# Performance work log

Measured on AMD Instinct MI355X. Metric: run time of the kernel, lower is better.

Reference implementation:

```python
import jax, jax.numpy as jnp
import numpy as np

N_ATOMS, N_BONDS, B = 3072, 12288, 64
D, H, L = 256, 8, 4
AF, BF = 74, 12
HD = D // H
EPS = 1e-5


def layer_norm(x, g, b):
    m = jnp.mean(x, -1, keepdims=True)
    v = jnp.mean((x - m) ** 2, -1, keepdims=True)
    return (x - m) / jnp.sqrt(v + EPS) * g + b


def mha(x, in_w, in_b, out_w, out_b, mask=None):
    # torch nn.MultiheadAttention with packed in_proj, batch of 1 sequence
    n = x.shape[0]
    qkv = x @ in_w.T + in_b                      # [n, 3D]
    q, k, v = jnp.split(qkv, 3, axis=-1)
    q = q.reshape(n, H, HD)
    k = k.reshape(n, H, HD)
    v = v.reshape(n, H, HD)
    scores = jnp.einsum('qhd,khd->hqk', q, k) / jnp.asarray(np.sqrt(HD), x.dtype)
    if mask is not None:
        scores = jnp.where(mask[None], scores, jnp.asarray(-1e9, x.dtype))
    att = jax.nn.softmax(scores, axis=-1)
    out = jnp.einsum('hqk,khd->qhd', att, v).reshape(n, D)
    return out @ out_w.T + out_b


def setup_inputs() -> dict:
    key = jax.random.key(0)
    ks = jax.random.split(key, 12)
    s = 0.05
    return {
        'atom_features': jax.random.normal(ks[0], (N_ATOMS, AF), jnp.float32),
        'bond_features': jax.random.normal(ks[1], (N_BONDS, BF), jnp.float32),
        'edge_indices': jax.random.randint(ks[2], (2, N_BONDS), 0, N_ATOMS),
        'batch_idx': jnp.sort(jax.random.randint(ks[3], (N_ATOMS,), 0, B)),
        'atom_w': jax.random.normal(ks[4], (D, AF), jnp.float32) * s,
        'atom_b': jnp.zeros((D,), jnp.float32),
        'bond_w': jax.random.normal(ks[5], (D, BF), jnp.float32) * s,
        'bond_b': jnp.zeros((D,), jnp.float32),
        'conv_w': jax.random.normal(ks[6], (L, D, 2 * D), jnp.float32) * s,
        'conv_b': jnp.zeros((L, D), jnp.float32),
        'attn_in_w': jax.random.normal(ks[7], (L, 3 * D, D), jnp.float32) * s,
        'attn_in_b': jnp.zeros((L, 3 * D), jnp.float32),
        'attn_out_w': jax.random.normal(ks[8], (L, D, D), jnp.float32) * s,
        'attn_out_b': jnp.zeros((L, D), jnp.float32),
        'ln_g': jnp.ones((L, D), jnp.float32),
        'ln_b': jnp.zeros((L, D), jnp.float32),
        'gattn_in_w': jax.random.normal(ks[9], (3 * D, D), jnp.float32) * s,
        'gattn_in_b': jnp.zeros((3 * D,), jnp.float32),
        'gattn_out_w': jax.random.normal(ks[10], (D, D), jnp.float32) * s,
        'gattn_out_b': jnp.zeros((D,), jnp.float32),
        'gn_g': jnp.ones((D,), jnp.float32),
        'gn_b': jnp.zeros((D,), jnp.float32),
    }


def reference(atom_features, bond_features, edge_indices, batch_idx,
              atom_w, atom_b, bond_w, bond_b, conv_w, conv_b,
              attn_in_w, attn_in_b, attn_out_w, attn_out_b, ln_g, ln_b,
              gattn_in_w, gattn_in_b, gattn_out_w, gattn_out_b, gn_g, gn_b):
    atom_h = atom_features @ atom_w.T + atom_b       # [N, D]
    bond_h = bond_features @ bond_w.T + bond_b       # [E, D]
    src, tgt = edge_indices[0], edge_indices[1]
    for i in range(L):
        # gather -> concat -> linear -> relu -> scatter-add
        messages = jnp.concatenate([atom_h[src] + bond_h, atom_h[tgt]], axis=-1)
        messages = jax.nn.relu(messages @ conv_w[i].T + conv_b[i])
        aggregated = jnp.zeros_like(atom_h).at[tgt].add(messages)
        # self-attention over all atoms as a single sequence (as in source)
        attended = mha(atom_h, attn_in_w[i], attn_in_b[i], attn_out_w[i], attn_out_b[i])
        atom_h = layer_norm(atom_h + aggregated + attended, ln_g[i], ln_b[i])
    # per-graph pooled attention == full attention masked to same-graph pairs
    same_graph = batch_idx[:, None] == batch_idx[None, :]
    pooled = mha(atom_h, gattn_in_w, gattn_in_b, gattn_out_w, gattn_out_b, mask=same_graph)
    pooled = layer_norm(pooled, gn_g, gn_b)
    sums = jax.ops.segment_sum(pooled, batch_idx, num_segments=B)
    counts = jax.ops.segment_sum(jnp.ones((pooled.shape[0],), pooled.dtype), batch_idx, num_segments=B)
    return sums / jnp.maximum(counts, 1.0)[:, None]   # empty graphs -> zeros, as in source
```

## Files before the change

### kernel.cpp

```cpp
#include <hip/hip_runtime.h>
#include <hip/hip_bf16.h>
#include <math.h>

#define NATOMS 3072
#define NBONDS 12288
#define NGRAPH 64
#define DIM 256
#define NH 8
#define HDIM 32
#define NLAYER 4
#define AFD 74
#define BFD 12
#define LNEPS 1e-5f
#define HSZ (NATOMS * HDIM)

typedef __attribute__((ext_vector_type(8))) short bf16x8;
typedef __attribute__((ext_vector_type(4))) short s16x4;
typedef __attribute__((ext_vector_type(4))) float f32x4;

static __device__ __forceinline__ short f2bf(float x) {
  union { float f; unsigned u; } v; v.f = x;
  unsigned r = v.u + 0x7fff + ((v.u >> 16) & 1);
  return (short)(r >> 16);
}

static __device__ __forceinline__ size_t afrag(int m, int c) {
  return ((size_t)(m >> 4) * 8 + (c >> 5)) * 512 + (m & 15) * 32 + (c & 31);
}

__global__ __launch_bounds__(256) void repack_w_kernel(
    const float* __restrict__ W, short* __restrict__ out, int kcShift, int n8) {
  const int o8 = blockIdx.x * 256 + threadIdx.x;
  if (o8 >= n8) return;
  const int g = o8 & 3, lq = (o8 >> 2) & 15, sub = (o8 >> 6) & 3;
  const int chunk = o8 >> 8;
  const int kc = chunk & ((1 << kcShift) - 1);
  const int nt = chunk >> kcShift;
  const int K = 32 << kcShift;
  const int n = nt * 64 + sub * 16 + lq;
  const int c = kc * 32 + g * 8;
  const float* src = W + (size_t)n * K + c;
  bf16x8 o;
  #pragma unroll
  for (int j = 0; j < 8; ++j) o[j] = f2bf(src[j]);
  ((bf16x8*)out)[o8] = o;
}

__global__ __launch_bounds__(256) void atom_proj_kernel(
    const float* __restrict__ feat, const float* __restrict__ w,
    const float* __restrict__ b, float* __restrict__ out, short* __restrict__ outbf) {
  __shared__ float x[AFD];
  const int a = blockIdx.x, t = threadIdx.x;
  if (t < AFD) x[t] = feat[a * AFD + t];
  __syncthreads();
  float acc = b[t];
  const float* wr = w + t * AFD;
  for (int k = 0; k < AFD; ++k) acc = fmaf(wr[k], x[k], acc);
  out[a * DIM + t] = acc;
  outbf[afrag(a, t)] = f2bf(acc);
}

__global__ __launch_bounds__(256) void bond_proj_kernel(
    const float* __restrict__ feat, const float* __restrict__ w,
    const float* __restrict__ b, short* __restrict__ outbf) {
  __shared__ float x[BFD];
  const int e = blockIdx.x, t = threadIdx.x;
  if (t < BFD) x[t] = feat[e * BFD + t];
  __syncthreads();
  float acc = b[t];
  const float* wr = w + t * BFD;
  #pragma unroll
  for (int k = 0; k < BFD; ++k) acc = fmaf(wr[k], x[k], acc);
  outbf[afrag(e, t)] = f2bf(acc);
}

__global__ __launch_bounds__(256) void hist_kernel(
    const int* __restrict__ tgt, int* __restrict__ counts) {
  const int e = blockIdx.x * 256 + threadIdx.x;
  if (e < NBONDS) atomicAdd(&counts[tgt[e]], 1);
}

__global__ __launch_bounds__(256) void scan_kernel(
    const int* __restrict__ counts, int* __restrict__ rowptr,
    int* __restrict__ cursor) {
  __shared__ int part[256];
  const int t = threadIdx.x;
  int loc[12], s = 0;
  #pragma unroll
  for (int j = 0; j < 12; ++j) { loc[j] = counts[t * 12 + j]; s += loc[j]; }
  part[t] = s;
  __syncthreads();
  for (int o = 1; o < 256; o <<= 1) {
    const int v = (t >= o) ? part[t - o] : 0;
    __syncthreads();
    part[t] += v;
    __syncthreads();
  }
  int running = part[t] - s;
  #pragma unroll
  for (int j = 0; j < 12; ++j) {
    rowptr[t * 12 + j] = running;
    cursor[t * 12 + j] = running;
    running += loc[j];
  }
  if (t == 255) rowptr[NATOMS] = running;
}

__global__ __launch_bounds__(256) void scatter_kernel(
    const int* __restrict__ tgt, int* __restrict__ cursor,
    int* __restrict__ elist) {
  const int e = blockIdx.x * 256 + threadIdx.x;
  if (e < NBONDS) {
    const int pos = atomicAdd(&cursor[tgt[e]], 1);
    elist[pos] = e;
  }
}

__global__ __launch_bounds__(256) void msg_csr_kernel(
    const float* __restrict__ G1, const float* __restrict__ B1,
    const float* __restrict__ G2, const float* __restrict__ bias,
    const int* __restrict__ src, const int* __restrict__ rowptr,
    const int* __restrict__ elist, float* __restrict__ agg) {
  const int wv = threadIdx.x >> 6, lane = threadIdx.x & 63;
  const int t = blockIdx.x * 4 + wv;
  const int c = lane * 4;
  const float4 bb = *(const float4*)&bias[c];
  const float4 g2 = *(const float4*)&G2[(size_t)t * DIM + c];
  const float gx = g2.x + bb.x, gy = g2.y + bb.y, gz = g2.z + bb.z, gw = g2.w + bb.w;
  float4 acc = make_float4(0.f, 0.f, 0.f, 0.f);
  const int beg = rowptr[t], end = rowptr[t + 1];
  for (int j = beg; j < end; ++j) {
    const int e = elist[j];
    const int s = src[e];
    const float4 g1 = *(const float4*)&G1[(size_t)s * DIM + c];
    const float4 b1 = *(const float4*)&B1[(size_t)e * DIM + c];
    acc.x += fmaxf(g1.x + b1.x + gx, 0.f);
    acc.y += fmaxf(g1.y + b1.y + gy, 0.f);
    acc.z += fmaxf(g1.z + b1.z + gz, 0.f);
    acc.w += fmaxf(g1.w + b1.w + gw, 0.f);
  }
  *(float4*)&agg[(size_t)t * DIM + c] = acc;
}

template <int KCS, int KCB>
__global__ __launch_bounds__(256) void gemm_bt_kernel(
    const short* __restrict__ A, const short* __restrict__ W,
    const float* __restrict__ bias, float* __restrict__ Cf,
    short* __restrict__ Cbf, int ldc, short* __restrict__ Qb,
    short* __restrict__ Kff, short* __restrict__ Vtf, float qscale) {
  const int t = threadIdx.x;
  const int w = t >> 6, l = t & 63;
  const int lq = l & 15, g = l >> 4;
  const int mrow = blockIdx.x * 32 + (w & 1) * 16 + lq;
  const int nbase = blockIdx.y * 128 + (w >> 1) * 64;
  const int lof = lq * 32 + g * 8;
  const short* arow = A + (size_t)(mrow >> 4) * 8 * 512 + lof;
  const short* wch = W + ((size_t)(nbase >> 6) * KCS + KCB) * 2048 + lof;

  bf16x8 Xall[8];
  #pragma unroll
  for (int kc = 0; kc < 8; ++kc) Xall[kc] = *(const bf16x8*)(arow + kc * 512);

  bf16x8 Wb[2][4];
  #pragma unroll
  for (int sub = 0; sub < 4; ++sub)
    Wb[0][sub] = *(const bf16x8*)(wch + sub * 512);

  f32x4 acc[4] = {{0.f,0.f,0.f,0.f},{0.f,0.f,0.f,0.f},{0.f,0.f,0.f,0.f},{0.f,0.f,0.f,0.f}};
  #pragma unroll
  for (int kc = 0; kc < 8; ++kc) {
    const int cur = kc & 1, nxt = cur ^ 1;
    if (kc < 7) {
      #pragma unroll
      for (int sub = 0; sub < 4; ++sub)
        Wb[nxt][sub] = *(const bf16x8*)(wch + (kc + 1) * 2048 + sub * 512);
    }
    __builtin_amdgcn_sched_barrier(0);
    #pragma unroll
    for (int sub = 0; sub < 4; ++sub)
      acc[sub] = __builtin_amdgcn_mfma_f32_16x16x32_bf16(Wb[cur][sub], Xall[kc], acc[sub], 0, 0, 0);
  }

  const bool qkvmode = (Qb != nullptr);
  #pragma unroll
  for (int sub = 0; sub < 4; ++sub) {
    const int n = nbase + sub * 16 + g * 4;
    float4 v = make_float4(acc[sub][0], acc[sub][1], acc[sub][2], acc[sub][3]);
    if (bias) {
      const float4 b4 = *(const float4*)&bias[n];
      v.x += b4.x; v.y += b4.y; v.z += b4.z; v.w += b4.w;
    }
    if (qkvmode) {
      const int key = mrow;
      if (n < 256) {
        s16x4 o;
        o[0] = f2bf(v.x * qscale); o[1] = f2bf(v.y * qscale);
        o[2] = f2bf(v.z * qscale); o[3] = f2bf(v.w * qscale);
        *(s16x4*)&Qb[afrag(mrow, n)] = o;
      } else if (n < 512) {
        const int d = n - 256, h = d >> 5, dd = d & 31;
        const size_t base = (size_t)h * HSZ + (size_t)(key >> 6) * 2048 +
                            (size_t)((key & 63) >> 4) * 512 +
                            ((dd >> 3) * 16 + (key & 15)) * 8 + (dd & 7);
        s16x4 o;
        o[0] = f2bf(v.x); o[1] = f2bf(v.y); o[2] = f2bf(v.z); o[3] = f2bf(v.w);
        *(s16x4*)&Kff[base] = o;
      } else {
        const int d = n - 512, h = d >> 5;
        const int kt = (key & 63) >> 5, gg = (key & 31) >> 3, j = key & 7;
        const int hh = (d & 31) >> 4;
        const size_t base = (size_t)h * HSZ + (size_t)(key >> 6) * 2048 +
                            (size_t)(kt * 2 + hh) * 512 + gg * 128 + j;
        Vtf[base + (size_t)((d + 0) & 15) * 8] = f2bf(v.x);
        Vtf[base + (size_t)((d + 1) & 15) * 8] = f2bf(v.y);
        Vtf[base + (size_t)((d + 2) & 15) * 8] = f2bf(v.z);
        Vtf[base + (size_t)((d + 3) & 15) * 8] = f2bf(v.w);
      }
    } else {
      if (Cf) *(float4*)&Cf[(size_t)mrow * ldc + n] = v;
      if (Cbf) {
        s16x4 o;
        o[0] = f2bf(v.x); o[1] = f2bf(v.y); o[2] = f2bf(v.z); o[3] = f2bf(v.w);
        *(s16x4*)&Cbf[afrag(mrow, n)] = o;
      }
    }
  }
}

__global__ __launch_bounds__(256) void gemm_dual_kernel(
    const short* __restrict__ A, const short* __restrict__ W,
    float* __restrict__ G1, float* __restrict__ G2) {
  const int t = threadIdx.x;
  const int w = t >> 6, l = t & 63;
  const int lq = l & 15, g = l >> 4;
  const int mrow = blockIdx.x * 32 + (w & 1) * 16 + lq;
  const int nbase = blockIdx.y * 128 + (w >> 1) * 64;
  const int half = nbase >> 8;
  const int nl = nbase & 255;
  const int lof = lq * 32 + g * 8;
  const short* arow = A + (size_t)(mrow >> 4) * 8 * 512 + lof;
  const short* wch = W + ((size_t)(nl >> 6) * 16 + half * 8) * 2048 + lof;

  bf16x8 Xall[8];
  #pragma unroll
  for (int kc = 0; kc < 8; ++kc) Xall[kc] = *(const bf16x8*)(arow + kc * 512);

  bf16x8 Wb[2][4];
  #pragma unroll
  for (int sub = 0; sub < 4; ++sub)
    Wb[0][sub] = *(const bf16x8*)(wch + sub * 512);

  f32x4 acc[4] = {{0.f,0.f,0.f,0.f},{0.f,0.f,0.f,0.f},{0.f,0.f,0.f,0.f},{0.f,0.f,0.f,0.f}};
  #pragma unroll
  for (int kc = 0; kc < 8; ++kc) {
    const int cur = kc & 1, nxt = cur ^ 1;
    if (kc < 7) {
      #pragma unroll
      for (int sub = 0; sub < 4; ++sub)
        Wb[nxt][sub] = *(const bf16x8*)(wch + (kc + 1) * 2048 + sub * 512);
    }
    __builtin_amdgcn_sched_barrier(0);
    #pragma unroll
    for (int sub = 0; sub < 4; ++sub)
      acc[sub] = __builtin_amdgcn_mfma_f32_16x16x32_bf16(Wb[cur][sub], Xall[kc], acc[sub], 0, 0, 0);
  }

  float* C = half ? G2 : G1;
  #pragma unroll
  for (int sub = 0; sub < 4; ++sub) {
    const int n = nl + sub * 16 + g * 4;
    *(float4*)&C[(size_t)mrow * DIM + n] =
        make_float4(acc[sub][0], acc[sub][1], acc[sub][2], acc[sub][3]);
  }
}

template <bool RESID>
__global__ __launch_bounds__(256) void outproj_ln_kernel(
    const short* __restrict__ A, const short* __restrict__ W,
    const float* __restrict__ bias, const float* __restrict__ r1,
    const float* __restrict__ r2, const float* __restrict__ g,
    const float* __restrict__ b, float* __restrict__ outf,
    short* __restrict__ outbf) {
  __shared__ float Red[4][2][16];
  const int t = threadIdx.x;
  const int w = t >> 6, l = t & 63;
  const int lq = l & 15, gg = l >> 4;
  const int mtile = blockIdx.x;
  const int mrow = mtile * 16 + lq;
  const int nbase = w * 64;
  const int lof = lq * 32 + gg * 8;
  const short* arow = A + (size_t)mtile * 8 * 512 + lof;
  const short* wch = W + ((size_t)(nbase >> 6) * 8) * 2048 + lof;

  bf16x8 Xall[8];
  #pragma unroll
  for (int kc = 0; kc < 8; ++kc) Xall[kc] = *(const bf16x8*)(arow + kc * 512);

  bf16x8 Wb[2][4];
  #pragma unroll
  for (int sub = 0; sub < 4; ++sub)
    Wb[0][sub] = *(const bf16x8*)(wch + sub * 512);

  f32x4 acc[4] = {{0.f,0.f,0.f,0.f},{0.f,0.f,0.f,0.f},{0.f,0.f,0.f,0.f},{0.f,0.f,0.f,0.f}};
  #pragma unroll
  for (int kc = 0; kc < 8; ++kc) {
    const int cur = kc & 1, nxt = cur ^ 1;
    if (kc < 7) {
      #pragma unroll
      for (int sub = 0; sub < 4; ++sub)
        Wb[nxt][sub] = *(const bf16x8*)(wch + (kc + 1) * 2048 + sub * 512);
    }
    __builtin_amdgcn_sched_barrier(0);
    #pragma unroll
    for (int sub = 0; sub < 4; ++sub)
      acc[sub] = __builtin_amdgcn_mfma_f32_16x16x32_bf16(Wb[cur][sub], Xall[kc], acc[sub], 0, 0, 0);
  }

  float y[4][4];
  float sp = 0.f, qp = 0.f;
  #pragma unroll
  for (int sub = 0; sub < 4; ++sub) {
    const int n = nbase + sub * 16 + gg * 4;
    const float4 b4 = *(const float4*)&bias[n];
    float4 v = make_float4(acc[sub][0] + b4.x, acc[sub][1] + b4.y,
                           acc[sub][2] + b4.z, acc[sub][3] + b4.w);
    if (RESID) {
      const size_t idx = (size_t)mrow * DIM + n;
      const float4 a4 = *(const float4*)&r1[idx];
      const float4 c4 = *(const float4*)&r2[idx];
      v.x += a4.x + c4.x; v.y += a4.y + c4.y;
      v.z += a4.z + c4.z; v.w += a4.w + c4.w;
    }
    y[sub][0] = v.x; y[sub][1] = v.y; y[sub][2] = v.z; y[sub][3] = v.w;
    sp += (v.x + v.y) + (v.z + v.w);
    qp += (v.x * v.x + v.y * v.y) + (v.z * v.z + v.w * v.w);
  }
  sp += __shfl_xor(sp, 16); sp += __shfl_xor(sp, 32);
  qp += __shfl_xor(qp, 16); qp += __shfl_xor(qp, 32);
  if (l < 16) { Red[w][0][lq] = sp; Red[w][1][lq] = qp; }
  __syncthreads();
  const float s = Red[0][0][lq] + Red[1][0][lq] + Red[2][0][lq] + Red[3][0][lq];
  const float q = Red[0][1][lq] + Red[1][1][lq] + Red[2][1][lq] + Red[3][1][lq];
  const float mean = s * (1.f / 256.f);
  const float var = q * (1.f / 256.f) - mean * mean;
  const float rstd = rsqrtf(var + LNEPS);

  #pragma unroll
  for (int sub = 0; sub < 4; ++sub) {
    const int n = nbase + sub * 16 + gg * 4;
    const float4 g4 = *(const float4*)&g[n];
    const float4 b4 = *(const float4*)&b[n];
    float4 o;
    o.x = (y[sub][0] - mean) * rstd * g4.x + b4.x;
    o.y = (y[sub][1] - mean) * rstd * g4.y + b4.y;
    o.z = (y[sub][2] - mean) * rstd * g4.z + b4.z;
    o.w = (y[sub][3] - mean) * rstd * g4.w + b4.w;
    if (outf) *(float4*)&outf[(size_t)mrow * DIM + n] = o;
    if (outbf) {
      s16x4 ob;
      ob[0] = f2bf(o.x); ob[1] = f2bf(o.y); ob[2] = f2bf(o.z); ob[3] = f2bf(o.w);
      *(s16x4*)&outbf[afrag(mrow, n)] = ob;
    }
  }
}

template <bool MASKED>
__global__ __launch_bounds__(256) void attn_mfma_kernel(
    const short* __restrict__ Qb, const short* __restrict__ Kff,
    const short* __restrict__ Vtf, const int* __restrict__ bidx,
    short* __restrict__ outbf) {
  __shared__ short Ps[4][2][16 * 72];
  __shared__ float Comb[3][64][18];

  const int t = threadIdx.x;
  const int h = blockIdx.y;
  const int wid = t >> 6;
  const int l = t & 63;
  const int lq = l & 15;
  const int g = l >> 4;
  const int qt0 = blockIdx.x * 32;

  const bf16x8 Qf0 = *(const bf16x8*)(Qb + ((size_t)(qt0 >> 4) * 8 + h) * 512 + lq * 32 + g * 8);
  const bf16x8 Qf1 = *(const bf16x8*)(Qb + ((size_t)(qt0 >> 4) * 8 + 8 + h) * 512 + lq * 32 + g * 8);
  const int qg0 = MASKED ? bidx[qt0 + lq] : 0;
  const int qg1 = MASKED ? bidx[qt0 + 16 + lq] : 0;

  bf16x8 OnesF;
  #pragma unroll
  for (int j = 0; j < 8; ++j) OnesF[j] = (short)0x3F80;

  const short* kh = Kff + (size_t)h * HSZ + l * 8;
  const short* vh = Vtf + (size_t)h * HSZ + l * 8;

  f32x4 accO[2][2] = {{{0.f,0.f,0.f,0.f},{0.f,0.f,0.f,0.f}},
                      {{0.f,0.f,0.f,0.f},{0.f,0.f,0.f,0.f}}};
  f32x4 accL[2] = {{0.f,0.f,0.f,0.f},{0.f,0.f,0.f,0.f}};

  const int kbeg = wid * (NATOMS / 4);
  const int kend = kbeg + NATOMS / 4;

  bf16x8 Kf[2][4];
  bf16x8 Vf[2][4];
  int4 KBv[2][4];

#define LOAD_TILE(buf, kc)                                                      \
  {                                                                             \
    const size_t tb = (size_t)((kc) >> 6) * 2048;                               \
    _Pragma("unroll")                                                           \
    for (int kk = 0; kk < 4; ++kk)                                              \
      Kf[buf][kk] = *(const bf16x8*)(kh + tb + kk * 512);                       \
    _Pragma("unroll")                                                           \
    for (int ff = 0; ff < 4; ++ff)                                              \
      Vf[buf][ff] = *(const bf16x8*)(vh + tb + ff * 512);                       \
    if (MASKED) {                                                               \
      _Pragma("unroll")                                                         \
      for (int kk = 0; kk < 4; ++kk)                                            \
        KBv[buf][kk] = *(const int4*)(bidx + (kc) + kk * 16 + g * 4);           \
    }                                                                           \
  }

  LOAD_TILE(0, kbeg);

  for (int k0 = kbeg; k0 < kend; k0 += 128) {
    #pragma unroll
    for (int ph = 0; ph < 2; ++ph) {
      const int kcur = k0 + ph * 64;
      int kn = kcur + 64;
      if (kn >= kend) kn = kbeg;
      const int pb = ph ^ 1;
      LOAD_TILE(pb, kn);
      __builtin_amdgcn_sched_barrier(0);

      #pragma unroll
// ... 30 lines not shown
      for (int qt = 0; qt < 2; ++qt) {
        #pragma unroll
        for (int kt = 0; kt < 2; ++kt) {
          const bf16x8 Pf = *(const bf16x8*)&Ps[wid][qt][lq * 72 + kt * 32 + g * 8];
          #pragma unroll
          for (int hh = 0; hh < 2; ++hh)
            accO[qt][hh] = __builtin_amdgcn_mfma_f32_16x16x32_bf16(
                Vf[ph][kt * 2 + hh], Pf, accO[qt][hh], 0, 0, 0);
          accL[qt] = __builtin_amdgcn_mfma_f32_16x16x32_bf16(OnesF, Pf, accL[qt], 0, 0, 0);
        }
      }
    }
  }
#undef LOAD_TILE

  if (wid > 0) {
    #pragma unroll
    for (int qt = 0; qt < 2; ++qt) {
      Comb[wid - 1][l][qt * 9] = accL[qt][0];
      #pragma unroll
      for (int hh = 0; hh < 2; ++hh)
        #pragma unroll
        for (int r = 0; r < 4; ++r)
          Comb[wid - 1][l][qt * 9 + 1 + hh * 4 + r] = accO[qt][hh][r];
    }
  }
  __syncthreads();
  if (wid == 0) {
    #pragma unroll
    for (int qt = 0; qt < 2; ++qt) {
      float tot = accL[qt][0];
      #pragma unroll
      for (int w2 = 0; w2 < 3; ++w2) {
        tot += Comb[w2][l][qt * 9];
        #pragma unroll
        for (int hh = 0; hh < 2; ++hh)
          #pragma unroll
          for (int r = 0; r < 4; ++r)
            accO[qt][hh][r] += Comb[w2][l][qt * 9 + 1 + hh * 4 + r];
      }
      const float inv = 1.f / tot;
      const int qrow = qt0 + qt * 16 + lq;
      #pragma unroll
      for (int hh = 0; hh < 2; ++hh) {
        s16x4 o;
        #pragma unroll
        for (int r = 0; r < 4; ++r) o[r] = f2bf(accO[qt][hh][r] * inv);
        *(s16x4*)&outbf[afrag(qrow, h * HDIM + hh * 16 + g * 4)] = o;
      }
    }
  }
}

__global__ __launch_bounds__(256) void pool_seg_kernel(
    const float* __restrict__ pooled, const int* __restrict__ bidx,
    float* __restrict__ out) {
  const int b = blockIdx.x, t = threadIdx.x;
  __shared__ int se[2];
  if (t < 2) {
    const int target = b + t;
    int lo = 0, hi = NATOMS;
    while (lo < hi) {
      const int mid = (lo + hi) >> 1;
      if (bidx[mid] < target) lo = mid + 1; else hi = mid;
    }
    se[t] = lo;
  }
  __syncthreads();
  const int beg = se[0], end = se[1];
  float acc = 0.f;
  for (int a = beg; a < end; ++a) acc += pooled[(size_t)a * DIM + t];
  out[(size_t)b * DIM + t] = acc / fmaxf((float)(end - beg), 1.f);
}

extern "C" void kernel_launch(void* const* d_in, const int* in_sizes, int n_in,
                              void* d_out, int out_size, void* d_ws, size_t ws_size,
                              hipStream_t stream) {
  const float* atom_features = (const float*)d_in[0];
  const float* bond_features = (const float*)d_in[1];
  const int* edge_indices = (const int*)d_in[2];
  const int* batch_idx = (const int*)d_in[3];
  const float* atom_w = (const float*)d_in[4];
  const float* atom_b = (const float*)d_in[5];
  const float* bond_w = (const float*)d_in[6];
  const float* bond_b = (const float*)d_in[7];
  const float* conv_w = (const float*)d_in[8];
  const float* conv_b = (const float*)d_in[9];
  const float* attn_in_w = (const float*)d_in[10];
  const float* attn_in_b = (const float*)d_in[11];
  const float* attn_out_w = (const float*)d_in[12];
  const float* attn_out_b = (const float*)d_in[13];
  const float* ln_g = (const float*)d_in[14];
  const float* ln_b = (const float*)d_in[15];
  const float* gattn_in_w = (const float*)d_in[16];
  const float* gattn_in_b = (const float*)d_in[17];
  const float* gattn_out_w = (const float*)d_in[18];
  const float* gattn_out_b = (const float*)d_in[19];
  const float* gn_g = (const float*)d_in[20];
  const float* gn_b = (const float*)d_in[21];

  const float QSCALE = 0.17677669529663687f * 1.4426950408889634f;

  char* wsb = (char*)d_ws;
  size_t off = 0;
  auto alloc_f = [&](size_t n) { float* p = (float*)(wsb + off); off += n * 4; return p; };
  auto alloc_s = [&](size_t n) { short* p = (short*)(wsb + off); off += n * 2; return p; };
  auto alloc_i = [&](size_t n) { int* p = (int*)(wsb + off); off += n * 4; return p; };

  float* atom_h = alloc_f((size_t)NATOMS * DIM);
  float* B1     = alloc_f((size_t)NBONDS * DIM);
  float* G1     = alloc_f((size_t)NATOMS * DIM);
  float* G2     = alloc_f((size_t)NATOMS * DIM);
  float* agg    = alloc_f((size_t)NATOMS * DIM);
  short* atom_hb = alloc_s((size_t)NATOMS * DIM);
  short* bond_hb = alloc_s((size_t)NBONDS * DIM);
  short* q_b     = alloc_s((size_t)NATOMS * DIM);
  short* kff_b   = alloc_s((size_t)NATOMS * DIM);
  short* vtf_b   = alloc_s((size_t)NATOMS * DIM);
  short* att_b   = alloc_s((size_t)NATOMS * DIM);
  short* conv_wb = alloc_s((size_t)NLAYER * DIM * 2 * DIM);
  short* in_wb   = alloc_s((size_t)NLAYER * 3 * DIM * DIM);
  short* out_wb  = alloc_s((size_t)NLAYER * DIM * DIM);
  short* gin_wb  = alloc_s((size_t)3 * DIM * DIM);
  short* gout_wb = alloc_s((size_t)DIM * DIM);
  int* counts = alloc_i(NATOMS);
  int* rowptr = alloc_i(NATOMS + 1);
  int* cursor = alloc_i(NATOMS);
  int* elist  = alloc_i(NBONDS);
  if (ws_size < off) return;
  float* pooled = B1;

  const int* src = edge_indices;
  const int* tgt = edge_indices + NBONDS;

  hipMemsetAsync(counts, 0, NATOMS * sizeof(int), stream);
  hist_kernel<<<NBONDS / 256, 256, 0, stream>>>(tgt, counts);
  scan_kernel<<<1, 256, 0, stream>>>(counts, rowptr, cursor);
  scatter_kernel<<<NBONDS / 256, 256, 0, stream>>>(tgt, cursor, elist);

  auto repk = [&](const float* s, short* d, int kcShift, int N, int K) {
    const int n8 = N * K / 8;
    repack_w_kernel<<<(n8 + 255) / 256, 256, 0, stream>>>(s, d, kcShift, n8);
  };
  repk(conv_w, conv_wb, 4, NLAYER * DIM, 2 * DIM);
  repk(attn_in_w, in_wb, 3, NLAYER * 3 * DIM, DIM);
  repk(attn_out_w, out_wb, 3, NLAYER * DIM, DIM);
  repk(gattn_in_w, gin_wb, 3, 3 * DIM, DIM);
  repk(gattn_out_w, gout_wb, 3, DIM, DIM);

  atom_proj_kernel<<<NATOMS, 256, 0, stream>>>(atom_features, atom_w, atom_b, atom_h, atom_hb);
  bond_proj_kernel<<<NBONDS, 256, 0, stream>>>(bond_features, bond_w, bond_b, bond_hb);

  for (int i = 0; i < NLAYER; ++i) {
    const short* cw = conv_wb + (size_t)i * DIM * 2 * DIM;
    gemm_bt_kernel<16, 0><<<dim3(NBONDS / 32, 2), 256, 0, stream>>>(
        bond_hb, cw, nullptr, B1, nullptr, DIM, nullptr, nullptr, nullptr, 1.f);
    gemm_dual_kernel<<<dim3(NATOMS / 32, 4), 256, 0, stream>>>(atom_hb, cw, G1, G2);
    msg_csr_kernel<<<NATOMS / 4, 256, 0, stream>>>(
        G1, B1, G2, conv_b + (size_t)i * DIM, src, rowptr, elist, agg);
    gemm_bt_kernel<8, 0><<<dim3(NATOMS / 32, 6), 256, 0, stream>>>(
        atom_hb, in_wb + (size_t)i * 3 * DIM * DIM, attn_in_b + (size_t)i * 3 * DIM,
        nullptr, nullptr, 3 * DIM, q_b, kff_b, vtf_b, QSCALE);
    attn_mfma_kernel<false><<<dim3(NATOMS / 32, NH), 256, 0, stream>>>(
        q_b, kff_b, vtf_b, nullptr, att_b);
    outproj_ln_kernel<true><<<NATOMS / 16, 256, 0, stream>>>(
        att_b, out_wb + (size_t)i * DIM * DIM, attn_out_b + (size_t)i * DIM,
        atom_h, agg, ln_g + (size_t)i * DIM, ln_b + (size_t)i * DIM,
        atom_h, atom_hb);
  }

  gemm_bt_kernel<8, 0><<<dim3(NATOMS / 32, 6), 256, 0, stream>>>(
      atom_hb, gin_wb, gattn_in_b, nullptr, nullptr, 3 * DIM, q_b, kff_b, vtf_b, QSCALE);
  attn_mfma_kernel<true><<<dim3(NATOMS / 32, NH), 256, 0, stream>>>(
      q_b, kff_b, vtf_b, batch_idx, att_b);
  outproj_ln_kernel<false><<<NATOMS / 16, 256, 0, stream>>>(
      att_b, gout_wb, gattn_out_b, nullptr, nullptr, gn_g, gn_b,
      pooled, nullptr);

  pool_seg_kernel<<<NGRAPH, 256, 0, stream>>>(pooled, batch_idx, (float*)d_out);
}
```

Before: 366.0 us.

## Merge independent per-layer kernels into combined launches to cut launch count

Independent work is grouped into single launches that branch on block index. The five weight repacks become one kernel, and the atom/bond projections plus the histogram become another. Per layer, the bond GEMM, dual atom GEMM and QKV GEMM share one launch, and the attention and message aggregation share a mid kernel. This removes launch gaps and lets independent work fill the GPU concurrently, at the cost of mixing block types with different register and LDS needs, which may reduce occupancy.

Measured after the change: 313.4 us. 1.17x faster.

```diff
diff --git a/kernel.cpp b/kernel.cpp
--- a/kernel.cpp
+++ b/kernel.cpp
@@ -28,10 +28,38 @@
   return ((size_t)(m >> 4) * 8 + (c >> 5)) * 512 + (m & 15) * 32 + (c & 31);
 }
 
-__global__ __launch_bounds__(256) void repack_w_kernel(
-    const float* __restrict__ W, short* __restrict__ out, int kcShift, int n8) {
-  const int o8 = blockIdx.x * 256 + threadIdx.x;
-  if (o8 >= n8) return;
+static __device__ __forceinline__ void gemm_core(
+    const short* __restrict__ arow, const short* __restrict__ wch, f32x4* acc) {
+  bf16x8 Xall[8];
+  #pragma unroll
+  for (int kc = 0; kc < 8; ++kc) Xall[kc] = *(const bf16x8*)(arow + kc * 512);
+  bf16x8 Wb[2][4];
+  #pragma unroll
+  for (int sub = 0; sub < 4; ++sub) Wb[0][sub] = *(const bf16x8*)(wch + sub * 512);
+  #pragma unroll
+  for (int kc = 0; kc < 8; ++kc) {
+    const int cur = kc & 1, nxt = cur ^ 1;
+    if (kc < 7) {
+      #pragma unroll
+      for (int sub = 0; sub < 4; ++sub)
+        Wb[nxt][sub] = *(const bf16x8*)(wch + (kc + 1) * 2048 + sub * 512);
+    }
+    __builtin_amdgcn_sched_barrier(0);
+    #pragma unroll
+    for (int sub = 0; sub < 4; ++sub)
+      acc[sub] = __builtin_amdgcn_mfma_f32_16x16x32_bf16(Wb[cur][sub], Xall[kc], acc[sub], 0, 0, 0);
+  }
+}
+
+#define CONVW_N8 65536
+#define INW_N8   98304
+#define OUTW_N8  32768
+#define GINW_N8  24576
+#define GOUTW_N8 8192
+#define REPK_TOT (CONVW_N8 + INW_N8 + OUTW_N8 + GINW_N8 + GOUTW_N8)
+
+static __device__ __forceinline__ void repack_one(
+    const float* __restrict__ W, short* __restrict__ out, int kcShift, int o8) {
   const int g = o8 & 3, lq = (o8 >> 2) & 15, sub = (o8 >> 6) & 3;
   const int chunk = o8 >> 8;
   const int kc = chunk & ((1 << kcShift) - 1);
@@ -46,38 +74,56 @@
   ((bf16x8*)out)[o8] = o;
 }
 
-__global__ __launch_bounds__(256) void atom_proj_kernel(
-    const float* __restrict__ feat, const float* __restrict__ w,
-    const float* __restrict__ b, float* __restrict__ out, short* __restrict__ outbf) {
-  __shared__ float x[AFD];
-  const int a = blockIdx.x, t = threadIdx.x;
-  if (t < AFD) x[t] = feat[a * AFD + t];
-  __syncthreads();
-  float acc = b[t];
-  const float* wr = w + t * AFD;
-  for (int k = 0; k < AFD; ++k) acc = fmaf(wr[k], x[k], acc);
-  out[a * DIM + t] = acc;
-  outbf[afrag(a, t)] = f2bf(acc);
-}
-
-__global__ __launch_bounds__(256) void bond_proj_kernel(
-    const float* __restrict__ feat, const float* __restrict__ w,
-    const float* __restrict__ b, short* __restrict__ outbf) {
-  __shared__ float x[BFD];
-  const int e = blockIdx.x, t = threadIdx.x;
-  if (t < BFD) x[t] = feat[e * BFD + t];
-  __syncthreads();
-  float acc = b[t];
-  const float* wr = w + t * BFD;
-  #pragma unroll
-  for (int k = 0; k < BFD; ++k) acc = fmaf(wr[k], x[k], acc);
-  outbf[afrag(e, t)] = f2bf(acc);
-}
-
-__global__ __launch_bounds__(256) void hist_kernel(
-    const int* __restrict__ tgt, int* __restrict__ counts) {
-  const int e = blockIdx.x * 256 + threadIdx.x;
-  if (e < NBONDS) atomicAdd(&counts[tgt[e]], 1);
+__global__ __launch_bounds__(256) void repack_all_kernel(
+    const float* __restrict__ conv_w, const float* __restrict__ in_w,
+    const float* __restrict__ out_w, const float* __restrict__ gin_w,
+    const float* __restrict__ gout_w, short* __restrict__ conv_wb,
+    short* __restrict__ in_wb, short* __restrict__ out_wb,
+    short* __restrict__ gin_wb, short* __restrict__ gout_wb) {
+  int o8 = blockIdx.x * 256 + threadIdx.x;
+  if (o8 >= REPK_TOT) return;
+  if (o8 < CONVW_N8) { repack_one(conv_w, conv_wb, 4, o8); return; }
+  o8 -= CONVW_N8;
+  if (o8 < INW_N8) { repack_one(in_w, in_wb, 3, o8); return; }
+  o8 -= INW_N8;
+  if (o8 < OUTW_N8) { repack_one(out_w, out_wb, 3, o8); return; }
+  o8 -= OUTW_N8;
+  if (o8 < GINW_N8) { repack_one(gin_w, gin_wb, 3, o8); return; }
+  o8 -= GINW_N8;
+  repack_one(gout_w, gout_wb, 3, o8);
+}
+
+__global__ __launch_bounds__(256) void proj_hist_kernel(
+    const float* __restrict__ afeat, const float* __restrict__ aw,
+    const float* __restrict__ ab, float* __restrict__ atom_h,
+    short* __restrict__ atom_hb, const float* __restrict__ bfeat,
+    const float* __restrict__ bw, const float* __restrict__ bb,
+    short* __restrict__ bond_hb, const int* __restrict__ tgt,
+    int* __restrict__ counts) {
+  const int idx = blockIdx.x, t = threadIdx.x;
+  if (idx < NATOMS) {
+    __shared__ float x[AFD];
+    if (t < AFD) x[t] = afeat[idx * AFD + t];
+    __syncthreads();
+    float acc = ab[t];
+    const float* wr = aw + t * AFD;
+    for (int k = 0; k < AFD; ++k) acc = fmaf(wr[k], x[k], acc);
+    atom_h[idx * DIM + t] = acc;
+    atom_hb[afrag(idx, t)] = f2bf(acc);
+  } else if (idx < NATOMS + NBONDS) {
+    const int e = idx - NATOMS;
+    __shared__ float xb[BFD];
+    if (t < BFD) xb[t] = bfeat[e * BFD + t];
+    __syncthreads();
+    float acc = bb[t];
+    const float* wr = bw + t * BFD;
+    #pragma unroll
+    for (int k = 0; k < BFD; ++k) acc = fmaf(wr[k], xb[k], acc);
+    bond_hb[afrag(e, t)] = f2bf(acc);
+  } else {
+    const int e = (idx - NATOMS - NBONDS) * 256 + t;
+    if (e < NBONDS) atomicAdd(&counts[tgt[e]], 1);
+  }
 }
 
 __global__ __launch_bounds__(256) void scan_kernel(
@@ -116,82 +162,61 @@
   }
 }
 
-__global__ __launch_bounds__(256) void msg_csr_kernel(
-    const float* __restrict__ G1, const float* __restrict__ B1,
-    const float* __restrict__ G2, const float* __restrict__ bias,
-    const int* __restrict__ src, const int* __restrict__ rowptr,
-    const int* __restrict__ elist, float* __restrict__ agg) {
-  const int wv = threadIdx.x >> 6, lane = threadIdx.x & 63;
-  const int t = blockIdx.x * 4 + wv;
-  const int c = lane * 4;
-  const float4 bb = *(const float4*)&bias[c];
-  const float4 g2 = *(const float4*)&G2[(size_t)t * DIM + c];
-  const float gx = g2.x + bb.x, gy = g2.y + bb.y, gz = g2.z + bb.z, gw = g2.w + bb.w;
-  float4 acc = make_float4(0.f, 0.f, 0.f, 0.f);
-  const int beg = rowptr[t], end = rowptr[t + 1];
-  for (int j = beg; j < end; ++j) {
-    const int e = elist[j];
-    const int s = src[e];
-    const float4 g1 = *(const float4*)&G1[(size_t)s * DIM + c];
-    const float4 b1 = *(const float4*)&B1[(size_t)e * DIM + c];
-    acc.x += fmaxf(g1.x + b1.x + gx, 0.f);
-    acc.y += fmaxf(g1.y + b1.y + gy, 0.f);
-    acc.z += fmaxf(g1.z + b1.z + gz, 0.f);
-    acc.w += fmaxf(g1.w + b1.w + gw, 0.f);
-  }
-  *(float4*)&agg[(size_t)t * DIM + c] = acc;
-}
-
-template <int KCS, int KCB>
-__global__ __launch_bounds__(256) void gemm_bt_kernel(
-    const short* __restrict__ A, const short* __restrict__ W,
-    const float* __restrict__ bias, float* __restrict__ Cf,
-    short* __restrict__ Cbf, int ldc, short* __restrict__ Qb,
-    short* __restrict__ Kff, short* __restrict__ Vtf, float qscale) {
+__global__ __launch_bounds__(256) void layer_front_kernel(
+    const short* __restrict__ atom_hb, const short* __restrict__ bond_hb,
+    const short* __restrict__ cw, const short* __restrict__ inw,
+    const float* __restrict__ inb, float* __restrict__ B1,
+    float* __restrict__ G1, float* __restrict__ G2,
+    short* __restrict__ Qb, short* __restrict__ Kff, short* __restrict__ Vtf,
+    float qscale) {
   const int t = threadIdx.x;
   const int w = t >> 6, l = t & 63;
   const int lq = l & 15, g = l >> 4;
-  const int mrow = blockIdx.x * 32 + (w & 1) * 16 + lq;
-  const int nbase = blockIdx.y * 128 + (w >> 1) * 64;
   const int lof = lq * 32 + g * 8;
-  const short* arow = A + (size_t)(mrow >> 4) * 8 * 512 + lof;
-  const short* wch = W + ((size_t)(nbase >> 6) * KCS + KCB) * 2048 + lof;
-
-  bf16x8 Xall[8];
-  #pragma unroll
-  for (int kc = 0; kc < 8; ++kc) Xall[kc] = *(const bf16x8*)(arow + kc * 512);
-
-  bf16x8 Wb[2][4];
-  #pragma unroll
-  for (int sub = 0; sub < 4; ++sub)
-    Wb[0][sub] = *(const bf16x8*)(wch + sub * 512);
-
+  const int idx = blockIdx.x;
   f32x4 acc[4] = {{0.f,0.f,0.f,0.f},{0.f,0.f,0.f,0.f},{0.f,0.f,0.f,0.f},{0.f,0.f,0.f,0.f}};
-  #pragma unroll
-  for (int kc = 0; kc < 8; ++kc) {
-    const int cur = kc & 1, nxt = cur ^ 1;
-    if (kc < 7) {
-      #pragma unroll
-      for (int sub = 0; sub < 4; ++sub)
-        Wb[nxt][sub] = *(const bf16x8*)(wch + (kc + 1) * 2048 + sub * 512);
-    }
-    __builtin_amdgcn_sched_barrier(0);
-    #pragma unroll
-    for (int sub = 0; sub < 4; ++sub)
-      acc[sub] = __builtin_amdgcn_mfma_f32_16x16x32_bf16(Wb[cur][sub], Xall[kc], acc[sub], 0, 0, 0);
-  }
-
-  const bool qkvmode = (Qb != nullptr);
-  #pragma unroll
-  for (int sub = 0; sub < 4; ++sub) {
-    const int n = nbase + sub * 16 + g * 4;
-    float4 v = make_float4(acc[sub][0], acc[sub][1], acc[sub][2], acc[sub][3]);
-    if (bias) {
-      const float4 b4 = *(const float4*)&bias[n];
-      v.x += b4.x; v.y += b4.y; v.z += b4.z; v.w += b4.w;
-    }
-    if (qkvmode) {
-      const int key = mrow;
+
+  if (idx < 768) {
+    const int by = idx / 384, bx = idx % 384;
+    const int mrow = bx * 32 + (w & 1) * 16 + lq;
+    const int nbase = by * 128 + (w >> 1) * 64;
+    gemm_core(bond_hb + (size_t)(mrow >> 4) * 8 * 512 + lof,
+              cw + (size_t)(nbase >> 6) * 16 * 2048 + lof, acc);
+    #pragma unroll
+    for (int sub = 0; sub < 4; ++sub) {
+      const int n = nbase + sub * 16 + g * 4;
+      *(float4*)&B1[(size_t)mrow * DIM + n] =
+          make_float4(acc[sub][0], acc[sub][1], acc[sub][2], acc[sub][3]);
+    }
+  } else if (idx < 1152) {
+    const int i2 = idx - 768;
+    const int bx = i2 % 96, by = i2 / 96;
+    const int mrow = bx * 32 + (w & 1) * 16 + lq;
+    const int nbase = by * 128 + (w >> 1) * 64;
+    const int half = nbase >> 8, nl = nbase & 255;
+    gemm_core(atom_hb + (size_t)(mrow >> 4) * 8 * 512 + lof,
+              cw + ((size_t)(nl >> 6) * 16 + half * 8) * 2048 + lof, acc);
+    float* C = half ? G2 : G1;
+    #pragma unroll
+    for (int sub = 0; sub < 4; ++sub) {
+      const int n = nl + sub * 16 + g * 4;
+      *(float4*)&C[(size_t)mrow * DIM + n] =
+          make_float4(acc[sub][0], acc[sub][1], acc[sub][2], acc[sub][3]);
+    }
+  } else {
+    const int i3 = idx - 1152;
+    const int bx = i3 % 96, by = i3 / 96;
+    const int mrow = bx * 32 + (w & 1) * 16 + lq;
+    const int nbase = by * 128 + (w >> 1) * 64;
+    gemm_core(atom_hb + (size_t)(mrow >> 4) * 8 * 512 + lof,
+              inw + (size_t)(nbase >> 6) * 8 * 2048 + lof, acc);
+    const int key = mrow;
+    #pragma unroll
+    for (int sub = 0; sub < 4; ++sub) {
+      const int n = nbase + sub * 16 + g * 4;
+      const float4 b4 = *(const float4*)&inb[n];
+      float4 v = make_float4(acc[sub][0] + b4.x, acc[sub][1] + b4.y,
+                             acc[sub][2] + b4.z, acc[sub][3] + b4.w);
       if (n < 256) {
         s16x4 o;
         o[0] = f2bf(v.x * qscale); o[1] = f2bf(v.y * qscale);
@@ -216,169 +241,24 @@
         Vtf[base + (size_t)((d + 2) & 15) * 8] = f2bf(v.z);
         Vtf[base + (size_t)((d + 3) & 15) * 8] = f2bf(v.w);
       }
-    } else {
-      if (Cf) *(float4*)&Cf[(size_t)mrow * ldc + n] = v;
-      if (Cbf) {
-        s16x4 o;
-        o[0] = f2bf(v.x); o[1] = f2bf(v.y); o[2] = f2bf(v.z); o[3] = f2bf(v.w);
-        *(s16x4*)&Cbf[afrag(mrow, n)] = o;
-      }
-    }
-  }
-}
-
-__global__ __launch_bounds__(256) void gemm_dual_kernel(
-    const short* __restrict__ A, const short* __restrict__ W,
-    float* __restrict__ G1, float* __restrict__ G2) {
-  const int t = threadIdx.x;
-  const int w = t >> 6, l = t & 63;
-  const int lq = l & 15, g = l >> 4;
-  const int mrow = blockIdx.x * 32 + (w & 1) * 16 + lq;
-  const int nbase = blockIdx.y * 128 + (w >> 1) * 64;
-  const int half = nbase >> 8;
-  const int nl = nbase & 255;
-  const int lof = lq * 32 + g * 8;
-  const short* arow = A + (size_t)(mrow >> 4) * 8 * 512 + lof;
-  const short* wch = W + ((size_t)(nl >> 6) * 16 + half * 8) * 2048 + lof;
-
-  bf16x8 Xall[8];
-  #pragma unroll
-  for (int kc = 0; kc < 8; ++kc) Xall[kc] = *(const bf16x8*)(arow + kc * 512);
-
-  bf16x8 Wb[2][4];
-  #pragma unroll
-  for (int sub = 0; sub < 4; ++sub)
-    Wb[0][sub] = *(const bf16x8*)(wch + sub * 512);
-
-  f32x4 acc[4] = {{0.f,0.f,0.f,0.f},{0.f,0.f,0.f,0.f},{0.f,0.f,0.f,0.f},{0.f,0.f,0.f,0.f}};
-  #pragma unroll
-  for (int kc = 0; kc < 8; ++kc) {
-    const int cur = kc & 1, nxt = cur ^ 1;
-    if (kc < 7) {
-      #pragma unroll
-      for (int sub = 0; sub < 4; ++sub)
-        Wb[nxt][sub] = *(const bf16x8*)(wch + (kc + 1) * 2048 + sub * 512);
-    }
-    __builtin_amdgcn_sched_barrier(0);
-    #pragma unroll
-    for (int sub = 0; sub < 4; ++sub)
-      acc[sub] = __builtin_amdgcn_mfma_f32_16x16x32_bf16(Wb[cur][sub], Xall[kc], acc[sub], 0, 0, 0);
-  }
-
-  float* C = half ? G2 : G1;
-  #pragma unroll
-  for (int sub = 0; sub < 4; ++sub) {
-    const int n = nl + sub * 16 + g * 4;
-    *(float4*)&C[(size_t)mrow * DIM + n] =
-        make_float4(acc[sub][0], acc[sub][1], acc[sub][2], acc[sub][3]);
-  }
-}
-
-template <bool RESID>
-__global__ __launch_bounds__(256) void outproj_ln_kernel(
-    const short* __restrict__ A, const short* __restrict__ W,
-    const float* __restrict__ bias, const float* __restrict__ r1,
-    const float* __restrict__ r2, const float* __restrict__ g,
-    const float* __restrict__ b, float* __restrict__ outf,
-    short* __restrict__ outbf) {
-  __shared__ float Red[4][2][16];
-  const int t = threadIdx.x;
-  const int w = t >> 6, l = t & 63;
-  const int lq = l & 15, gg = l >> 4;
-  const int mtile = blockIdx.x;
-  const int mrow = mtile * 16 + lq;
-  const int nbase = w * 64;
-  const int lof = lq * 32 + gg * 8;
-  const short* arow = A + (size_t)mtile * 8 * 512 + lof;
-  const short* wch = W + ((size_t)(nbase >> 6) * 8) * 2048 + lof;
-
-  bf16x8 Xall[8];
-  #pragma unroll
-  for (int kc = 0; kc < 8; ++kc) Xall[kc] = *(const bf16x8*)(arow + kc * 512);
-
-  bf16x8 Wb[2][4];
-  #pragma unroll
-  for (int sub = 0; sub < 4; ++sub)
-    Wb[0][sub] = *(const bf16x8*)(wch + sub * 512);
-
-  f32x4 acc[4] = {{0.f,0.f,0.f,0.f},{0.f,0.f,0.f,0.f},{0.f,0.f,0.f,0.f},{0.f,0.f,0.f,0.f}};
-  #pragma unroll
-  for (int kc = 0; kc < 8; ++kc) {
-    const int cur = kc & 1, nxt = cur ^ 1;
-    if (kc < 7) {
-      #pragma unroll
-      for (int sub = 0; sub < 4; ++sub)
-        Wb[nxt][sub] = *(const bf16x8*)(wch + (kc + 1) * 2048 + sub * 512);
-    }
-    __builtin_amdgcn_sched_barrier(0);
-    #pragma unroll
-    for (int sub = 0; sub < 4; ++sub)
-      acc[sub] = __builtin_amdgcn_mfma_f32_16x16x32_bf16(Wb[cur][sub], Xall[kc], acc[sub], 0, 0, 0);
-  }
-
-  float y[4][4];
-  float sp = 0.f, qp = 0.f;
-  #pragma unroll
-  for (int sub = 0; sub < 4; ++sub) {
-    const int n = nbase + sub * 16 + gg * 4;
-    const float4 b4 = *(const float4*)&bias[n];
-    float4 v = make_float4(acc[sub][0] + b4.x, acc[sub][1] + b4.y,
-                           acc[sub][2] + b4.z, acc[sub][3] + b4.w);
-    if (RESID) {
-      const size_t idx = (size_t)mrow * DIM + n;
-      const float4 a4 = *(const float4*)&r1[idx];
-      const float4 c4 = *(const float4*)&r2[idx];
-      v.x += a4.x + c4.x; v.y += a4.y + c4.y;
-      v.z += a4.z + c4.z; v.w += a4.w + c4.w;
-    }
-    y[sub][0] = v.x; y[sub][1] = v.y; y[sub][2] = v.z; y[sub][3] = v.w;
-    sp += (v.x + v.y) + (v.z + v.w);
-    qp += (v.x * v.x + v.y * v.y) + (v.z * v.z + v.w * v.w);
-  }
-  sp += __shfl_xor(sp, 16); sp += __shfl_xor(sp, 32);
-  qp += __shfl_xor(qp, 16); qp += __shfl_xor(qp, 32);
-  if (l < 16) { Red[w][0][lq] = sp; Red[w][1][lq] = qp; }
-  __syncthreads();
-  const float s = Red[0][0][lq] + Red[1][0][lq] + Red[2][0][lq] + Red[3][0][lq];
-  const float q = Red[0][1][lq] + Red[1][1][lq] + Red[2][1][lq] + Red[3][1][lq];
-  const float mean = s * (1.f / 256.f);
-  const float var = q * (1.f / 256.f) - mean * mean;
-  const float rstd = rsqrtf(var + LNEPS);
-
-  #pragma unroll
-  for (int sub = 0; sub < 4; ++sub) {
-    const int n = nbase + sub * 16 + gg * 4;
-    const float4 g4 = *(const float4*)&g[n];
-    const float4 b4 = *(const float4*)&b[n];
-    float4 o;
-    o.x = (y[sub][0] - mean) * rstd * g4.x + b4.x;
-    o.y = (y[sub][1] - mean) * rstd * g4.y + b4.y;
-    o.z = (y[sub][2] - mean) * rstd * g4.z + b4.z;
-    o.w = (y[sub][3] - mean) * rstd * g4.w + b4.w;
-    if (outf) *(float4*)&outf[(size_t)mrow * DIM + n] = o;
-    if (outbf) {
-      s16x4 ob;
-      ob[0] = f2bf(o.x); ob[1] = f2bf(o.y); ob[2] = f2bf(o.z); ob[3] = f2bf(o.w);
-      *(s16x4*)&outbf[afrag(mrow, n)] = ob;
     }
   }
 }
 
 template <bool MASKED>
-__global__ __launch_bounds__(256) void attn_mfma_kernel(
-    const short* __restrict__ Qb, const short* __restrict__ Kff,
-    const short* __restrict__ Vtf, const int* __restrict__ bidx,
-    short* __restrict__ outbf) {
+static __device__ __forceinline__ void attn_body(
+    int qtile, int h, const short* __restrict__ Qb,
+    const short* __restrict__ Kff, const short* __restrict__ Vtf,
+    const int* __restrict__ bidx, short* __restrict__ outbf) {
   __shared__ short Ps[4][2][16 * 72];
   __shared__ float Comb[3][64][18];
 
   const int t = threadIdx.x;
-  const int h = blockIdx.y;
   const int wid = t >> 6;
   const int l = t & 63;
   const int lq = l & 15;
   const int g = l >> 4;
-  const int qt0 = blockIdx.x * 32;
+  const int qt0 = qtile * 32;
 
   const bf16x8 Qf0 = *(const bf16x8*)(Qb + ((size_t)(qt0 >> 4) * 8 + h) * 512 + lq * 32 + g * 8);
   const bf16x8 Qf1 = *(const bf16x8*)(Qb + ((size_t)(qt0 >> 4) * 8 + 8 + h) * 512 + lq * 32 + g * 8);
@@ -515,6 +395,169 @@
   }
 }
 
+static __device__ __forceinline__ void msg_body(
+    int blk, const float* __restrict__ G1, const float* __restrict__ B1,
+    const float* __restrict__ G2, const float* __restrict__ bias,
+    const int* __restrict__ src, const int* __restrict__ rowptr,
+    const int* __restrict__ elist, float* __restrict__ agg) {
+  const int wv = threadIdx.x >> 6, lane = threadIdx.x & 63;
+  const int t = blk * 4 + wv;
+  const int c = lane * 4;
+  const float4 bb = *(const float4*)&bias[c];
+  const float4 g2 = *(const float4*)&G2[(size_t)t * DIM + c];
+  const float gx = g2.x + bb.x, gy = g2.y + bb.y, gz = g2.z + bb.z, gw = g2.w + bb.w;
+  float4 acc = make_float4(0.f, 0.f, 0.f, 0.f);
+  const int beg = rowptr[t], end = rowptr[t + 1];
+  for (int j = beg; j < end; ++j) {
+    const int e = elist[j];
+    const int s = src[e];
+    const float4 g1 = *(const float4*)&G1[(size_t)s * DIM + c];
+    const float4 b1 = *(const float4*)&B1[(size_t)e * DIM + c];
+    acc.x += fmaxf(g1.x + b1.x + gx, 0.f);
+    acc.y += fmaxf(g1.y + b1.y + gy, 0.f);
+    acc.z += fmaxf(g1.z + b1.z + gz, 0.f);
+    acc.w += fmaxf(g1.w + b1.w + gw, 0.f);
+  }
+  *(float4*)&agg[(size_t)t * DIM + c] = acc;
+}
+
+__global__ __launch_bounds__(256) void layer_mid_kernel(
+    const short* __restrict__ Qb, const short* __restrict__ Kff,
+    const short* __restrict__ Vtf, short* __restrict__ att_b,
+    const float* __restrict__ G1, const float* __restrict__ B1,
+    const float* __restrict__ G2, const float* __restrict__ bias,
+    const int* __restrict__ src, const int* __restrict__ rowptr,
+    const int* __restrict__ elist, float* __restrict__ agg) {
+  const int idx = blockIdx.x;
+  if (idx < 768) {
+    attn_body<false>(idx % 96, idx / 96, Qb, Kff, Vtf, nullptr, att_b);
+  } else {
+    msg_body(idx - 768, G1, B1, G2, bias, src, rowptr, elist, agg);
+  }
+}
+
+template <bool MASKED>
+__global__ __launch_bounds__(256) void attn_mfma_kernel(
+    const short* __restrict__ Qb, const short* __restrict__ Kff,
+    const short* __restrict__ Vtf, const int* __restrict__ bidx,
+    short* __restrict__ outbf) {
+  attn_body<MASKED>(blockIdx.x, blockIdx.y, Qb, Kff, Vtf, bidx, outbf);
+}
+
+__global__ __launch_bounds__(256) void gemm_qkv_kernel(
+    const short* __restrict__ A, const short* __restrict__ W,
+    const float* __restrict__ bias, short* __restrict__ Qb,
+    short* __restrict__ Kff, short* __restrict__ Vtf, float qscale) {
+  const int t = threadIdx.x;
+  const int w = t >> 6, l = t & 63;
+  const int lq = l & 15, g = l >> 4;
+  const int mrow = blockIdx.x * 32 + (w & 1) * 16 + lq;
+  const int nbase = blockIdx.y * 128 + (w >> 1) * 64;
+  const int lof = lq * 32 + g * 8;
+  f32x4 acc[4] = {{0.f,0.f,0.f,0.f},{0.f,0.f,0.f,0.f},{0.f,0.f,0.f,0.f},{0.f,0.f,0.f,0.f}};
+  gemm_core(A + (size_t)(mrow >> 4) * 8 * 512 + lof,
+            W + (size_t)(nbase >> 6) * 8 * 2048 + lof, acc);
+  const int key = mrow;
+  #pragma unroll
+  for (int sub = 0; sub < 4; ++sub) {
+    const int n = nbase + sub * 16 + g * 4;
+    const float4 b4 = *(const float4*)&bias[n];
+    float4 v = make_float4(acc[sub][0] + b4.x, acc[sub][1] + b4.y,
+                           acc[sub][2] + b4.z, acc[sub][3] + b4.w);
+    if (n < 256) {
+      s16x4 o;
+      o[0] = f2bf(v.x * qscale); o[1] = f2bf(v.y * qscale);
+      o[2] = f2bf(v.z * qscale); o[3] = f2bf(v.w * qscale);
+      *(s16x4*)&Qb[afrag(mrow, n)] = o;
+    } else if (n < 512) {
+      const int d = n - 256, h = d >> 5, dd = d & 31;
+      const size_t base = (size_t)h * HSZ + (size_t)(key >> 6) * 2048 +
+                          (size_t)((key & 63) >> 4) * 512 +
+                          ((dd >> 3) * 16 + (key & 15)) * 8 + (dd & 7);
+      s16x4 o;
+      o[0] = f2bf(v.x); o[1] = f2bf(v.y); o[2] = f2bf(v.z); o[3] = f2bf(v.w);
+      *(s16x4*)&Kff[base] = o;
+    } else {
+      const int d = n - 512, h = d >> 5;
+      const int kt = (key & 63) >> 5, gg = (key & 31) >> 3, j = key & 7;
+      const int hh = (d & 31) >> 4;
+      const size_t base = (size_t)h * HSZ + (size_t)(key >> 6) * 2048 +
+                          (size_t)(kt * 2 + hh) * 512 + gg * 128 + j;
+      Vtf[base + (size_t)((d + 0) & 15) * 8] = f2bf(v.x);
+      Vtf[base + (size_t)((d + 1) & 15) * 8] = f2bf(v.y);
+      Vtf[base + (size_t)((d + 2) & 15) * 8] = f2bf(v.z);
+      Vtf[base + (size_t)((d + 3) & 15) * 8] = f2bf(v.w);
+    }
+  }
+}
+
+template <bool RESID>
+__global__ __launch_bounds__(256) void outproj_ln_kernel(
+    const short* __restrict__ A, const short* __restrict__ W,
+    const float* __restrict__ bias, const float* __restrict__ r1,
+    const float* __restrict__ r2, const float* __restrict__ g,
+    const float* __restrict__ b, float* __restrict__ outf,
+    short* __restrict__ outbf) {
+  __shared__ float Red[4][2][16];
+  const int t = threadIdx.x;
+  const int w = t >> 6, l = t & 63;
+  const int lq = l & 15, gg = l >> 4;
+  const int mtile = blockIdx.x;
+  const int mrow = mtile * 16 + lq;
+  const int nbase = w * 64;
+  const int lof = lq * 32 + gg * 8;
+  f32x4 acc[4] = {{0.f,0.f,0.f,0.f},{0.f,0.f,0.f,0.f},{0.f,0.f,0.f,0.f},{0.f,0.f,0.f,0.f}};
+  gemm_core(A + (size_t)mtile * 8 * 512 + lof,
+            W + (size_t)(nbase >> 6) * 8 * 2048 + lof, acc);
+
+  float y[4][4];
+  float sp = 0.f, qp = 0.f;
+  #pragma unroll
+  for (int sub = 0; sub < 4; ++sub) {
+    const int n = nbase + sub * 16 + gg * 4;
+    const float4 b4 = *(const float4*)&bias[n];
+    float4 v = make_float4(acc[sub][0] + b4.x, acc[sub][1] + b4.y,
+                           acc[sub][2] + b4.z, acc[sub][3] + b4.w);
+    if (RESID) {
+      const size_t i2 = (size_t)mrow * DIM + n;
+      const float4 a4 = *(const float4*)&r1[i2];
+      const float4 c4 = *(const float4*)&r2[i2];
+      v.x += a4.x + c4.x; v.y += a4.y + c4.y;
+      v.z += a4.z + c4.z; v.w += a4.w + c4.w;
+    }
+    y[sub][0] = v.x; y[sub][1] = v.y; y[sub][2] = v.z; y[sub][3] = v.w;
+    sp += (v.x + v.y) + (v.z + v.w);
+    qp += (v.x * v.x + v.y * v.y) + (v.z * v.z + v.w * v.w);
+  }
+  sp += __shfl_xor(sp, 16); sp += __shfl_xor(sp, 32);
+  qp += __shfl_xor(qp, 16); qp += __shfl_xor(qp, 32);
+  if (l < 16) { Red[w][0][lq] = sp; Red[w][1][lq] = qp; }
+  __syncthreads();
+  const float s = Red[0][0][lq] + Red[1][0][lq] + Red[2][0][lq] + Red[3][0][lq];
+  const float q = Red[0][1][lq] + Red[1][1][lq] + Red[2][1][lq] + Red[3][1][lq];
+  const float mean = s * (1.f / 256.f);
+  const float var = q * (1.f / 256.f) - mean * mean;
+  const float rstd = rsqrtf(var + LNEPS);
+
+  #pragma unroll
+  for (int sub = 0; sub < 4; ++sub) {
+    const int n = nbase + sub * 16 + gg * 4;
+    const float4 g4 = *(const float4*)&g[n];
+    const float4 b4 = *(const float4*)&b[n];
+    float4 o;
+    o.x = (y[sub][0] - mean) * rstd * g4.x + b4.x;
+    o.y = (y[sub][1] - mean) * rstd * g4.y + b4.y;
+    o.z = (y[sub][2] - mean) * rstd * g4.z + b4.z;
+    o.w = (y[sub][3] - mean) * rstd * g4.w + b4.w;
+    if (outf) *(float4*)&outf[(size_t)mrow * DIM + n] = o;
+    if (outbf) {
+      s16x4 ob;
+      ob[0] = f2bf(o.x); ob[1] = f2bf(o.y); ob[2] = f2bf(o.z); ob[3] = f2bf(o.w);
+      *(s16x4*)&outbf[afrag(mrow, n)] = ob;
+    }
+  }
+}
+
 __global__ __launch_bounds__(256) void pool_seg_kernel(
     const float* __restrict__ pooled, const int* __restrict__ bidx,
     float* __restrict__ out) {
@@ -597,44 +640,32 @@
   const int* tgt = edge_indices + NBONDS;
 
   hipMemsetAsync(counts, 0, NATOMS * sizeof(int), stream);
-  hist_kernel<<<NBONDS / 256, 256, 0, stream>>>(tgt, counts);
+  proj_hist_kernel<<<NATOMS + NBONDS + NBONDS / 256, 256, 0, stream>>>(
+      atom_features, atom_w, atom_b, atom_h, atom_hb,
+      bond_features, bond_w, bond_b, bond_hb, tgt, counts);
   scan_kernel<<<1, 256, 0, stream>>>(counts, rowptr, cursor);
   scatter_kernel<<<NBONDS / 256, 256, 0, stream>>>(tgt, cursor, elist);
-
-  auto repk = [&](const float* s, short* d, int kcShift, int N, int K) {
-    const int n8 = N * K / 8;
-    repack_w_kernel<<<(n8 + 255) / 256, 256, 0, stream>>>(s, d, kcShift, n8);
-  };
-  repk(conv_w, conv_wb, 4, NLAYER * DIM, 2 * DIM);
-  repk(attn_in_w, in_wb, 3, NLAYER * 3 * DIM, DIM);
-  repk(attn_out_w, out_wb, 3, NLAYER * DIM, DIM);
-  repk(gattn_in_w, gin_wb, 3, 3 * DIM, DIM);
-  repk(gattn_out_w, gout_wb, 3, DIM, DIM);
-
-  atom_proj_kernel<<<NATOMS, 256, 0, stream>>>(atom_features, atom_w, atom_b, atom_h, atom_hb);
-  bond_proj_kernel<<<NBONDS, 256, 0, stream>>>(bond_features, bond_w, bond_b, bond_hb);
+  repack_all_kernel<<<(REPK_TOT + 255) / 256, 256, 0, stream>>>(
+      conv_w, attn_in_w, attn_out_w, gattn_in_w, gattn_out_w,
+      conv_wb, in_wb, out_wb, gin_wb, gout_wb);
 
   for (int i = 0; i < NLAYER; ++i) {
-    const short* cw = conv_wb + (size_t)i * DIM * 2 * DIM;
-    gemm_bt_kernel<16, 0><<<dim3(NBONDS / 32, 2), 256, 0, stream>>>(
-        bond_hb, cw, nullptr, B1, nullptr, DIM, nullptr, nullptr, nullptr, 1.f);
-    gemm_dual_kernel<<<dim3(NATOMS / 32, 4), 256, 0, stream>>>(atom_hb, cw, G1, G2);
-    msg_csr_kernel<<<NATOMS / 4, 256, 0, stream>>>(
-        G1, B1, G2, conv_b + (size_t)i * DIM, src, rowptr, elist, agg);
-    gemm_bt_kernel<8, 0><<<dim3(NATOMS / 32, 6), 256, 0, stream>>>(
-        atom_hb, in_wb + (size_t)i * 3 * DIM * DIM, attn_in_b + (size_t)i * 3 * DIM,
-        nullptr, nullptr, 3 * DIM, q_b, kff_b, vtf_b, QSCALE);
-    attn_mfma_kernel<false><<<dim3(NATOMS / 32, NH), 256, 0, stream>>>(
-        q_b, kff_b, vtf_b, nullptr, att_b);
+    layer_front_kernel<<<1728, 256, 0, stream>>>(
+        atom_hb, bond_hb, conv_wb + (size_t)i * DIM * 2 * DIM,
+        in_wb + (size_t)i * 3 * DIM * DIM, attn_in_b + (size_t)i * 3 * DIM,
+        B1, G1, G2, q_b, kff_b, vtf_b, QSCALE);
+    layer_mid_kernel<<<1536, 256, 0, stream>>>(
+        q_b, kff_b, vtf_b, att_b, G1, B1, G2, conv_b + (size_t)i * DIM,
+        src, rowptr, elist, agg);
     outproj_ln_kernel<true><<<NATOMS / 16, 256, 0, stream>>>(
         att_b, out_wb + (size_t)i * DIM * DIM, attn_out_b + (size_t)i * DIM,
         atom_h, agg, ln_g + (size_t)i * DIM, ln_b + (size_t)i * DIM,
         atom_h, atom_hb);
   }
 
-  gemm_bt_kernel<8, 0><<<dim3(NATOMS / 32, 6), 256, 0, stream>>>(
-      atom_hb, gin_wb, gattn_in_b, nullptr, nullptr, 3 * DIM, q_b, kff_b, vtf_b, QSCALE);
-  attn_mfma_kernel<true><<<dim3(NATOMS / 32, NH), 256, 0, stream>>>(
+  gemm_qkv_kernel<<<dim3(96, 6), 256, 0, stream>>>(
+      atom_hb, gin_wb, gattn_in_b, q_b, kff_b, vtf_b, QSCALE);
+  attn_mfma_kernel<true><<<dim3(96, 8), 256, 0, stream>>>(
       q_b, kff_b, vtf_b, batch_idx, att_b);
   outproj_ln_kernel<false><<<NATOMS / 16, 256, 0, stream>>>(
       att_b, gout_wb, gattn_out_b, nullptr, nullptr, gn_g, gn_b,
```
